# Performance work log

Measured on AMD Instinct MI355X. Metric: run time of the kernel, lower is better.

## Reference

```python
import jax, jax.numpy as jnp
import numpy as np

B, L, HID = 4, 2048, 896
NH, NKV, HD = 14, 2, 64
GROUPS = NH // NKV  # 7
ROPE_THETA = 1000000.0


def _rotate_half(x):
    x1, x2 = x[..., : HD // 2], x[..., HD // 2 :]
    return jnp.concatenate([-x2, x1], axis=-1)


def setup_inputs() -> dict:
    key = jax.random.key(0)
    ks = jax.random.split(key, 8)
    x = jax.random.normal(ks[0], (B, L, HID), dtype=jnp.float32)
    # RoPE tables (HF convention: freqs repeated twice along last dim)
    inv_freq = 1.0 / (ROPE_THETA ** (np.arange(0, HD, 2, dtype=np.float32) / HD))
    t = np.arange(L, dtype=np.float32)
    freqs = np.outer(t, inv_freq)  # [L, HD/2]
    emb = np.concatenate([freqs, freqs], axis=-1)  # [L, HD]
    cos = jnp.asarray(np.cos(emb))[None, None]  # [1,1,L,HD]
    sin = jnp.asarray(np.sin(emb))[None, None]
    # Causal additive mask (finite large negative for numerical safety)
    causal = jnp.tril(jnp.ones((L, L), dtype=bool))
    mask = jnp.where(causal, 0.0, -1e9).astype(jnp.float32)[None, None]
    s = 0.02
    wq = jax.random.normal(ks[1], (NH * HD, HID), dtype=jnp.float32) * s
    bq = jax.random.normal(ks[2], (NH * HD,), dtype=jnp.float32) * s
    wk = jax.random.normal(ks[3], (NKV * HD, HID), dtype=jnp.float32) * s
    bk = jax.random.normal(ks[4], (NKV * HD,), dtype=jnp.float32) * s
    wv = jax.random.normal(ks[5], (NKV * HD, HID), dtype=jnp.float32) * s
    bv = jax.random.normal(ks[6], (NKV * HD,), dtype=jnp.float32) * s
    wo = jax.random.normal(ks[7], (HID, NH * HD), dtype=jnp.float32) * s
    return {"x": x, "cos": cos, "sin": sin, "mask": mask,
            "wq": wq, "bq": bq, "wk": wk, "bk": bk, "wv": wv, "bv": bv, "wo": wo}


def reference(x, cos, sin, mask, wq, bq, wk, bk, wv, bv, wo):
    b, l, _ = x.shape
    q = (x @ wq.T + bq).reshape(b, l, NH, HD).transpose(0, 2, 1, 3)   # [B,NH,L,HD]
    k = (x @ wk.T + bk).reshape(b, l, NKV, HD).transpose(0, 2, 1, 3)  # [B,NKV,L,HD]
    v = (x @ wv.T + bv).reshape(b, l, NKV, HD).transpose(0, 2, 1, 3)
    # RoPE
    q = q * cos + _rotate_half(q) * sin
    k = k * cos + _rotate_half(k) * sin
    # GQA expansion of KV heads
    k = jnp.repeat(k, GROUPS, axis=1)  # [B,NH,L,HD]
    v = jnp.repeat(v, GROUPS, axis=1)
    scale = 1.0 / jnp.sqrt(jnp.float32(HD))
    attn = jnp.einsum("bhqd,bhkd->bhqk", q, k) * scale + mask
    attn = jax.nn.softmax(attn, axis=-1)
    out = jnp.einsum("bhqk,bhkd->bhqd", attn, v)
    out = out.transpose(0, 2, 1, 3).reshape(b, l, NH * HD)
    return out @ wo.T
```

## Files before the change

### kernel.cpp

```cpp
#include <hip/hip_runtime.h>
#include <hip/hip_bf16.h>
#include <math.h>

#define B 4
#define L 2048
#define HID 896
#define NH 14
#define NKV 2
#define HD 64
#define GROUPS 7
#define QCOLS (NH * HD)
#define KCOLS (NKV * HD)
#define ROWS (B * L)
#define QKVS 1152

typedef __attribute__((ext_vector_type(8))) short bf16x8;
typedef __attribute__((ext_vector_type(4))) short bf16x4;
typedef __attribute__((ext_vector_type(4))) float f32x4;
typedef unsigned short ushort_t;
typedef unsigned int uint_t;

__device__ inline short f2bf(float f) {
  union { __hip_bfloat16 h; short s; } u;
  u.h = __float2bfloat16(f);
  return u.s;
}

__device__ inline uint_t pack2_bf16(float a, float b) {
  return (uint_t)(ushort_t)f2bf(a) | ((uint_t)(ushort_t)f2bf(b) << 16);
}

#if defined(__HIP_DEVICE_COMPILE__)
__device__ inline f32x4 mfma16(bf16x4 a, bf16x4 b, f32x4 c) {
  return __builtin_amdgcn_mfma_f32_16x16x16bf16_1k(a, b, c, 0, 0, 0);
}
#define EXP2(x) __builtin_amdgcn_exp2f(x)
#else
__device__ inline f32x4 mfma16(bf16x4 a, bf16x4 b, f32x4 c) { return c; }
#define EXP2(x) exp2f(x)
#endif

__device__ inline void gload_lds16(const void* g, void* l) {
  __builtin_amdgcn_global_load_lds(
      (const __attribute__((address_space(1))) unsigned int*)g,
      (__attribute__((address_space(3))) unsigned int*)l, 16, 0, 0);
}

__device__ inline void cast8(const float* __restrict__ in,
                             short* __restrict__ out) {
  const float4* p = (const float4*)in;
  float4 a = p[0], b = p[1];
  short s[8];
  s[0] = f2bf(a.x); s[1] = f2bf(a.y); s[2] = f2bf(a.z); s[3] = f2bf(a.w);
  s[4] = f2bf(b.x); s[5] = f2bf(b.y); s[6] = f2bf(b.z); s[7] = f2bf(b.w);
  *(bf16x8*)out = *(bf16x8*)s;
}

#define NX8 (ROWS * HID / 8)
#define NQ8 (QCOLS * HID / 8)
#define NK8 (KCOLS * HID / 8)
#define PREP_TOTAL (NX8 + NQ8 + NK8 + NK8 + NQ8 + QKVS)

__global__ void prep_kernel(const float* __restrict__ x,
                            const float* __restrict__ wq,
                            const float* __restrict__ wk,
                            const float* __restrict__ wv,
                            const float* __restrict__ wo,
                            const float* __restrict__ bq,
                            const float* __restrict__ bk,
                            const float* __restrict__ bv,
                            short* __restrict__ xb,
                            short* __restrict__ wqkvb,
                            short* __restrict__ wob,
                            float* __restrict__ bqkv) {
  int i = blockIdx.x * blockDim.x + threadIdx.x;
  if (i < NX8) { cast8(x + (size_t)i * 8, xb + (size_t)i * 8); return; }
  i -= NX8;
  if (i < NQ8) { cast8(wq + (size_t)i * 8, wqkvb + (size_t)i * 8); return; }
  i -= NQ8;
  if (i < NK8) {
    cast8(wk + (size_t)i * 8, wqkvb + (size_t)QCOLS * HID + (size_t)i * 8);
    return;
  }
  i -= NK8;
  if (i < NK8) {
    cast8(wv + (size_t)i * 8,
          wqkvb + (size_t)(QCOLS + KCOLS) * HID + (size_t)i * 8);
    return;
  }
  i -= NK8;
  if (i < NQ8) { cast8(wo + (size_t)i * 8, wob + (size_t)i * 8); return; }
  i -= NQ8;
  if (i < QKVS) {
    float v;
    if (i < QCOLS) v = bq[i];
    else if (i < QCOLS + KCOLS) v = bk[i - QCOLS];
    else v = bv[i - QCOLS - KCOLS];
    bqkv[i] = v;
  }
}

#define GTM 128
#define GTN 128
#define GTK 32
#define QSCALE 0.18033688011112042f

template <bool ROPE>
__global__ __launch_bounds__(256) void gemm_bf16_kernel(
    const short* __restrict__ A, const short* __restrict__ W,
    const float* __restrict__ bias, float* __restrict__ C,
    short* __restrict__ Cb, const float* __restrict__ cosp,
    const float* __restrict__ sinp, int M, int N, int K) {
  __shared__ short As[2][GTM * GTK];
  __shared__ short Bs[2][GTN * GTK];

  const int tid = threadIdx.x;
  const int wave = tid >> 6;
  const int lane = tid & 63;
  const int l15 = lane & 15;
  const int quad = lane >> 4;
  const int m0 = blockIdx.y * GTM;
  const int n0 = blockIdx.x * GTN;
  const int wm = (wave >> 1) * 64;
  const int wn = (wave & 1) * 64;

  f32x4 acc[4][4] = {};

  const int c0 = tid, c1 = tid + 256;
  const int r0 = c0 >> 2, g0 = (c0 & 3) ^ ((r0 >> 1) & 3);
  const int r1 = c1 >> 2, g1 = (c1 & 3) ^ ((r1 >> 1) & 3);
  const short* Ag0 = A + (size_t)(m0 + r0) * K + g0 * 8;
  const short* Ag1 = A + (size_t)(m0 + r1) * K + g1 * 8;
  const short* Wg0 = W + (size_t)(n0 + r0) * K + g0 * 8;
  const short* Wg1 = W + (size_t)(n0 + r1) * K + g1 * 8;

  const int goff = ((quad ^ ((l15 >> 1) & 3)) * 8);

  const int nsteps = K / GTK;

  auto stage = [&](int step, int bufi) {
    const int k0 = step * GTK;
    gload_lds16(Ag0 + k0, &As[bufi][c0 * 8]);
    gload_lds16(Ag1 + k0, &As[bufi][c1 * 8]);
    gload_lds16(Wg0 + k0, &Bs[bufi][c0 * 8]);
    gload_lds16(Wg1 + k0, &Bs[bufi][c1 * 8]);
  };

  stage(0, 0);
  __syncthreads();

  int cur = 0;
  for (int step = 0; step < nsteps; ++step) {
    if (step + 1 < nsteps) stage(step + 1, cur ^ 1);

    bf16x8 af[4], bfr[4];
#pragma unroll
    for (int i = 0; i < 4; ++i)
      af[i] = *(bf16x8*)(&As[cur][(wm + i * 16 + l15) * GTK + goff]);
#pragma unroll
    for (int j = 0; j < 4; ++j)
      bfr[j] = *(bf16x8*)(&Bs[cur][(wn + j * 16 + l15) * GTK + goff]);
#pragma unroll
    for (int i = 0; i < 4; ++i)
#pragma unroll
      for (int j = 0; j < 4; ++j)
        acc[i][j] = __builtin_amdgcn_mfma_f32_16x16x32_bf16(af[i], bfr[j],
                                                            acc[i][j], 0, 0, 0);

    __syncthreads();
    cur ^= 1;
  }

  const int col0 = n0 + wn + l15;
  if (ROPE) {
    const int hw = (n0 + wn) >> 6;
    float bv[4];
#pragma unroll
    for (int j = 0; j < 4; ++j) bv[j] = bias[col0 + 16 * j];
    if (hw < NH + NKV) {
      const float sc = (hw < NH) ? QSCALE : 1.0f;
#pragma unroll
      for (int i = 0; i < 4; ++i) {
        const int rowb = m0 + wm + i * 16 + quad * 4;
#pragma unroll
        for (int r = 0; r < 4; ++r) {
          const int row = rowb + r;
          const int l = row & (L - 1);
          const float* cp = cosp + l * HD + l15;
          const float* sp = sinp + l * HD + l15;
#pragma unroll
          for (int j = 0; j < 2; ++j) {
            const float cv = cp[16 * j];
            const float sv = sp[16 * j];
            const float a = acc[i][j][r] + bv[j];
            const float b2 = acc[i][j + 2][r] + bv[j + 2];
            Cb[(size_t)row * N + col0 + 16 * j] = f2bf((a * cv - b2 * sv) * sc);
            Cb[(size_t)row * N + col0 + 16 * j + 32] =
                f2bf((b2 * cv + a * sv) * sc);
          }
        }
      }
    } else {
#pragma unroll
      for (int j = 0; j < 4; ++j)
#pragma unroll
        for (int i = 0; i < 4; ++i) {
          const int rowb = m0 + wm + i * 16 + quad * 4;
#pragma unroll
          for (int r = 0; r < 4; ++r)
            Cb[(size_t)(rowb + r) * N + col0 + 16 * j] =
                f2bf(acc[i][j][r] + bv[j]);
        }
    }
  } else {
#pragma unroll
    for (int j = 0; j < 4; ++j) {
      const int col = col0 + 16 * j;
      const float bv = bias ? bias[col] : 0.f;
#pragma unroll
      for (int i = 0; i < 4; ++i) {
        const int rowb = m0 + wm + i * 16 + quad * 4;
#pragma unroll
        for (int r = 0; r < 4; ++r)
          C[(size_t)(rowb + r) * N + col] = acc[i][j][r] + bv;
      }
    }
  }
}

#define BK 64
#define QSTRIP 128
#define NSTRIPS (L / QSTRIP)

__global__ __launch_bounds__(512, 4) void attn_mfma_kernel(
    const ushort_t* __restrict__ qkv, ushort_t* __restrict__ ctx) {
  const int strip = (NSTRIPS - 1) - blockIdx.y;
  const int h = blockIdx.x % NH;
  const int b = blockIdx.x / NH;
  const int kvh = h / GROUPS;
  const int tid = threadIdx.x;
  const int wave = tid >> 6;
  const int lane = tid & 63;
  const int l15 = lane & 15;
  const int quad = lane >> 4;

  const int lt = 2 * strip + 1;
  const int qrb = strip * QSTRIP + wave * 16;
  const int myDiag = (qrb + 15) >> 6;

  __shared__ short Kt[2][BK * 64];
  __shared__ short Vt[2][BK * 64];

  bf16x8 qf[2];
  {
    const ushort_t* qp = qkv + (size_t)(b * L + qrb + l15) * QKVS + h * HD;
    qf[0] = *(const bf16x8*)(qp + quad * 8);
    qf[1] = *(const bf16x8*)(qp + 32 + quad * 8);
  }

  float m = -INFINITY, lsum = 0.f;
  f32x4 o[4] = {};

  const ushort_t* kb = qkv + (size_t)(b * L) * QKVS + QCOLS + kvh * HD;
  const ushort_t* vb = kb + KCOLS;

  const int skey = tid >> 3;
  const int sgr = tid & 7;
  const int ksw = skey * 64 + (sgr ^ (skey & 7)) * 8;
  const int vd = tid & 63;
  const int vsw = vd * 64 + ((wave ^ (vd & 7)) * 8);

  uint4 kr, vrp;

  auto load_tile = [&](int j0) {
    kr = *(const uint4*)(kb + (size_t)(j0 + skey) * QKVS + sgr * 8);
    const ushort_t* vp = vb + (size_t)(j0 + wave * 8) * QKVS + vd;
    ushort_t vr[8];
#pragma unroll
    for (int s2 = 0; s2 < 8; ++s2) vr[s2] = vp[(size_t)s2 * QKVS];
    vrp.x = (uint_t)vr[0] | ((uint_t)vr[1] << 16);
    vrp.y = (uint_t)vr[2] | ((uint_t)vr[3] << 16);
    vrp.z = (uint_t)vr[4] | ((uint_t)vr[5] << 16);
    vrp.w = (uint_t)vr[6] | ((uint_t)vr[7] << 16);
  };
  auto store_tile = [&](int bufi) {
    *(uint4*)(&Kt[bufi][ksw]) = kr;
    *(uint4*)(&Vt[bufi][vsw]) = vrp;
  };

  load_tile(0);
  store_tile(0);
  __syncthreads();

  const int dl7 = l15 & 7;
  const int qh = quad >> 1;
  const int qoff = (quad & 1) * 4;

  for (int t = 0; t <= lt; ++t) {
    const int j0 = t * BK;
    const int cur = t & 1;
    if (t < lt) load_tile(j0 + BK);

    if (t <= myDiag) {
      const short* Kb = Kt[cur];
      const short* Vb = Vt[cur];

      f32x4 St[4];
      __builtin_amdgcn_s_setprio(1);
#pragma unroll
      for (int tt = 0; tt < 4; ++tt) {
        const int key = tt * 16 + l15;
        const short* krow = Kb + key * 64;
        bf16x8 k0 = *(const bf16x8*)(krow + (quad ^ (key & 7)) * 8);
        bf16x8 k1 = *(const bf16x8*)(krow + ((4 + quad) ^ (key & 7)) * 8);
        f32x4 a = {};
        a = __builtin_amdgcn_mfma_f32_16x16x32_bf16(k0, qf[0], a, 0, 0, 0);
        a = __builtin_amdgcn_mfma_f32_16x16x32_bf16(k1, qf[1], a, 0, 0, 0);
        St[tt] = a;
      }
      __builtin_amdgcn_s_setprio(0);

      float s[16];
      if (t == myDiag) {
        const int limq = qrb + l15 - j0 - quad * 4;
#pragma unroll
        for (int tt = 0; tt < 4; ++tt)
#pragma unroll
          for (int r = 0; r < 4; ++r)
            s[tt * 4 + r] = (tt * 16 + r <= limq) ? St[tt][r] : -1e30f;
      } else {
#pragma unroll
        for (int tt = 0; tt < 4; ++tt)
#pragma unroll
          for (int r = 0; r < 4; ++r) s[tt * 4 + r] = St[tt][r];
      }

      float mt = fmaxf(s[0], s[1]);
#pragma unroll
      for (int i = 2; i < 16; ++i) mt = fmaxf(mt, s[i]);
      float pl[16], psl = 0.f;
#pragma unroll
      for (int i = 0; i < 16; ++i) {
        pl[i] = EXP2(s[i] - mt);
        psl += pl[i];
      }
      float mg = fmaxf(mt, __shfl_xor(mt, 16));
      mg = fmaxf(mg, __shfl_xor(mg, 32));

      float f;
      if (__all(mg <= m + 8.0f)) {
        f = EXP2(mt - m);
        lsum += psl * f;
      } else {
        const float mn = fmaxf(m, mg);
        const float al = EXP2(m - mn);
        f = EXP2(mt - mn);
        m = mn;
        lsum = lsum * al + psl * f;
#pragma unroll
        for (int c = 0; c < 4; ++c)
#pragma unroll
          for (int r = 0; r < 4; ++r) o[c][r] *= al;
      }

      uint_t pk[8];
#pragma unroll
      for (int tt = 0; tt < 4; ++tt) {
        pk[2 * tt] = pack2_bf16(pl[4 * tt] * f, pl[4 * tt + 1] * f);
        pk[2 * tt + 1] = pack2_bf16(pl[4 * tt + 2] * f, pl[4 * tt + 3] * f);
      }

      __builtin_amdgcn_s_setprio(1);
#pragma unroll
      for (int c = 0; c < 4; ++c) {
        const short* vrow = Vb + (c * 16 + l15) * 64;
#pragma unroll
        for (int tt = 0; tt < 4; ++tt) {
          const int g = tt * 2 + qh;
          union { bf16x4 v; uint2 u; } vfu;
          vfu.u = *(const uint2*)(vrow + ((g ^ dl7) * 8) + qoff);
          union { bf16x4 v; uint_t u[2]; } pa;
          pa.u[0] = pk[2 * tt];
          pa.u[1] = pk[2 * tt + 1];
          o[c] = mfma16(vfu.v, pa.v, o[c]);
        }
      }
      __builtin_amdgcn_s_setprio(0);
    }

    if (t < lt) store_tile(cur ^ 1);
    __syncthreads();
  }

  float s1 = lsum;
  s1 += __shfl_xor(s1, 16);
  s1 += __shfl_xor(s1, 32);
  const float inv = 1.0f / s1;
  ushort_t* cb = ctx + (size_t)(b * L) * QCOLS + h * HD;
#pragma unroll
  for (int c = 0; c < 4; ++c) {
    uint_t w[2];
    w[0] = pack2_bf16(o[c][0] * inv, o[c][1] * inv);
    w[1] = pack2_bf16(o[c][2] * inv, o[c][3] * inv);
    *(uint2*)(cb + (size_t)(qrb + l15) * QCOLS + c * 16 + quad * 4) =
        *(uint2*)w;
  }
}

extern "C" void kernel_launch(void* const* d_in, const int* in_sizes, int n_in,
                              void* d_out, int out_size, void* d_ws,
                              size_t ws_size, hipStream_t stream) {
  const float* x = (const float*)d_in[0];
  const float* cosp = (const float*)d_in[1];
  const float* sinp = (const float*)d_in[2];
  const float* wq = (const float*)d_in[4];
  const float* bq = (const float*)d_in[5];
  const float* wk = (const float*)d_in[6];
  const float* bk = (const float*)d_in[7];
  const float* wv = (const float*)d_in[8];
  const float* bv = (const float*)d_in[9];
  const float* wo = (const float*)d_in[10];
  float* out = (float*)d_out;

  char* ws = (char*)d_ws;
  ushort_t* qkvb = (ushort_t*)ws;
  ws += (size_t)ROWS * QKVS * 2;
  short* xb = (short*)ws;
  ws += (size_t)ROWS * HID * 2;
  short* wqkvb = (short*)ws;
  ws += (size_t)QKVS * HID * 2;
  short* wob = (short*)ws;
  ws += (size_t)HID * QCOLS * 2;
  ushort_t* ctxb = (ushort_t*)ws;
  ws += (size_t)ROWS * QCOLS * 2;
  float* bqkv = (float*)ws;
  ws += QKVS * 4;

  prep_kernel<<<(PREP_TOTAL + 255) / 256, 256, 0, stream>>>(
      x, wq, wk, wv, wo, bq, bk, bv, xb, wqkvb, wob, bqkv);

  gemm_bf16_kernel<true><<<dim3(QKVS / GTN, ROWS / GTM), 256, 0, stream>>>(
      xb, wqkvb, bqkv, nullptr, (short*)qkvb, cosp, sinp, ROWS, QKVS, HID);

  attn_mfma_kernel<<<dim3(NH * B, NSTRIPS), 512, 0, stream>>>(qkvb, ctxb);

  gemm_bf16_kernel<false><<<dim3(HID / GTN, ROWS / GTM), 256, 0, stream>>>(
      (const short*)ctxb, wob, nullptr, out, nullptr, nullptr, nullptr, ROWS,
      HID, QCOLS);
}
```

Baseline: 229.5 us.

## Use single-wave 64x64 GEMM blocks with vmcnt waits instead of barriers

Restructures both projection GEMMs so each block is one 64-lane wave computing a 64x64 tile, in place of four waves sharing a 128x128 tile. With a single wave, __syncthreads is replaced by explicit s_waitcnt vmcnt waits on the async global-to-LDS loads, keeping the double-buffer overlap. This gives many more blocks (better CU fill for the small N dimensions) and removes barrier cost, but halves per-block data reuse so global/L2 traffic per FLOP rises.

```diff
diff --git a/kernel.cpp b/kernel.cpp
--- a/kernel.cpp
+++ b/kernel.cpp
@@ -100,80 +100,79 @@
   }
 }
 
-#define GTM 128
-#define GTN 128
 #define GTK 32
 #define QSCALE 0.18033688011112042f
 
 template <bool ROPE>
-__global__ __launch_bounds__(256) void gemm_bf16_kernel(
+__global__ __launch_bounds__(64) void gemm_bf16_kernel(
     const short* __restrict__ A, const short* __restrict__ W,
     const float* __restrict__ bias, float* __restrict__ C,
     short* __restrict__ Cb, const float* __restrict__ cosp,
     const float* __restrict__ sinp, int M, int N, int K) {
-  __shared__ short As[2][GTM * GTK];
-  __shared__ short Bs[2][GTN * GTK];
+  __shared__ short As[2][64 * 32];
+  __shared__ short Bs[2][64 * 32];
 
   const int tid = threadIdx.x;
-  const int wave = tid >> 6;
-  const int lane = tid & 63;
-  const int l15 = lane & 15;
-  const int quad = lane >> 4;
-  const int m0 = blockIdx.y * GTM;
-  const int n0 = blockIdx.x * GTN;
-  const int wm = (wave >> 1) * 64;
-  const int wn = (wave & 1) * 64;
+  const int l15 = tid & 15;
+  const int quad = tid >> 4;
+  const int m0 = blockIdx.y * 64;
+  const int n0 = blockIdx.x * 64;
 
   f32x4 acc[4][4] = {};
 
-  const int c0 = tid, c1 = tid + 256;
-  const int r0 = c0 >> 2, g0 = (c0 & 3) ^ ((r0 >> 1) & 3);
-  const int r1 = c1 >> 2, g1 = (c1 & 3) ^ ((r1 >> 1) & 3);
-  const short* Ag0 = A + (size_t)(m0 + r0) * K + g0 * 8;
-  const short* Ag1 = A + (size_t)(m0 + r1) * K + g1 * 8;
-  const short* Wg0 = W + (size_t)(n0 + r0) * K + g0 * 8;
-  const short* Wg1 = W + (size_t)(n0 + r1) * K + g1 * 8;
-
-  const int goff = ((quad ^ ((l15 >> 1) & 3)) * 8);
-
+  const short* Asrc[4];
+  const short* Wsrc[4];
+#pragma unroll
+  for (int j = 0; j < 4; ++j) {
+    const int r = 16 * j + (tid >> 2);
+    const int g = (tid & 3) ^ ((r >> 1) & 3);
+    Asrc[j] = A + (size_t)(m0 + r) * K + g * 8;
+    Wsrc[j] = W + (size_t)(n0 + r) * K + g * 8;
+  }
+
+  const int goff = (quad ^ ((l15 >> 1) & 3)) * 8;
   const int nsteps = K / GTK;
 
   auto stage = [&](int step, int bufi) {
     const int k0 = step * GTK;
-    gload_lds16(Ag0 + k0, &As[bufi][c0 * 8]);
-    gload_lds16(Ag1 + k0, &As[bufi][c1 * 8]);
-    gload_lds16(Wg0 + k0, &Bs[bufi][c0 * 8]);
-    gload_lds16(Wg1 + k0, &Bs[bufi][c1 * 8]);
+#pragma unroll
+    for (int j = 0; j < 4; ++j)
+      gload_lds16(Asrc[j] + k0, &As[bufi][j * 512 + tid * 8]);
+#pragma unroll
+    for (int j = 0; j < 4; ++j)
+      gload_lds16(Wsrc[j] + k0, &Bs[bufi][j * 512 + tid * 8]);
   };
 
-  stage(0, 0);
-  __syncthreads();
-
-  int cur = 0;
-  for (int step = 0; step < nsteps; ++step) {
-    if (step + 1 < nsteps) stage(step + 1, cur ^ 1);
-
+  auto compute = [&](int bufi) {
     bf16x8 af[4], bfr[4];
 #pragma unroll
     for (int i = 0; i < 4; ++i)
-      af[i] = *(bf16x8*)(&As[cur][(wm + i * 16 + l15) * GTK + goff]);
+      af[i] = *(bf16x8*)(&As[bufi][(i * 16 + l15) * 32 + goff]);
 #pragma unroll
     for (int j = 0; j < 4; ++j)
-      bfr[j] = *(bf16x8*)(&Bs[cur][(wn + j * 16 + l15) * GTK + goff]);
+      bfr[j] = *(bf16x8*)(&Bs[bufi][(j * 16 + l15) * 32 + goff]);
 #pragma unroll
     for (int i = 0; i < 4; ++i)
 #pragma unroll
       for (int j = 0; j < 4; ++j)
         acc[i][j] = __builtin_amdgcn_mfma_f32_16x16x32_bf16(af[i], bfr[j],
                                                             acc[i][j], 0, 0, 0);
-
-    __syncthreads();
+  };
+
+  stage(0, 0);
+  int cur = 0;
+  for (int step = 0; step < nsteps - 1; ++step) {
+    stage(step + 1, cur ^ 1);
+    asm volatile("s_waitcnt vmcnt(8)" ::: "memory");
+    compute(cur);
     cur ^= 1;
   }
-
-  const int col0 = n0 + wn + l15;
+  asm volatile("s_waitcnt vmcnt(0)" ::: "memory");
+  compute(cur);
+
+  const int col0 = n0 + l15;
   if (ROPE) {
-    const int hw = (n0 + wn) >> 6;
+    const int hw = n0 >> 6;
     float bv[4];
 #pragma unroll
     for (int j = 0; j < 4; ++j) bv[j] = bias[col0 + 16 * j];
@@ -181,7 +180,7 @@
       const float sc = (hw < NH) ? QSCALE : 1.0f;
 #pragma unroll
       for (int i = 0; i < 4; ++i) {
-        const int rowb = m0 + wm + i * 16 + quad * 4;
+        const int rowb = m0 + i * 16 + quad * 4;
 #pragma unroll
         for (int r = 0; r < 4; ++r) {
           const int row = rowb + r;
@@ -205,7 +204,7 @@
       for (int j = 0; j < 4; ++j)
 #pragma unroll
         for (int i = 0; i < 4; ++i) {
-          const int rowb = m0 + wm + i * 16 + quad * 4;
+          const int rowb = m0 + i * 16 + quad * 4;
 #pragma unroll
           for (int r = 0; r < 4; ++r)
             Cb[(size_t)(rowb + r) * N + col0 + 16 * j] =
@@ -219,7 +218,7 @@
       const float bv = bias ? bias[col] : 0.f;
 #pragma unroll
       for (int i = 0; i < 4; ++i) {
-        const int rowb = m0 + wm + i * 16 + quad * 4;
+        const int rowb = m0 + i * 16 + quad * 4;
 #pragma unroll
         for (int r = 0; r < 4; ++r)
           C[(size_t)(rowb + r) * N + col] = acc[i][j][r] + bv;
@@ -439,12 +438,12 @@
   prep_kernel<<<(PREP_TOTAL + 255) / 256, 256, 0, stream>>>(
       x, wq, wk, wv, wo, bq, bk, bv, xb, wqkvb, wob, bqkv);
 
-  gemm_bf16_kernel<true><<<dim3(QKVS / GTN, ROWS / GTM), 256, 0, stream>>>(
+  gemm_bf16_kernel<true><<<dim3(QKVS / 64, ROWS / 64), 64, 0, stream>>>(
       xb, wqkvb, bqkv, nullptr, (short*)qkvb, cosp, sinp, ROWS, QKVS, HID);
 
   attn_mfma_kernel<<<dim3(NH * B, NSTRIPS), 512, 0, stream>>>(qkvb, ctxb);
 
-  gemm_bf16_kernel<false><<<dim3(HID / GTN, ROWS / GTM), 256, 0, stream>>>(
+  gemm_bf16_kernel<false><<<dim3(HID / 64, ROWS / 64), 64, 0, stream>>>(
       (const short*)ctxb, wob, nullptr, out, nullptr, nullptr, nullptr, ROWS,
       HID, QCOLS);
 }
```

New measurement: 260.7 us. 1.14x slower.
